# Kernel optimization log

Measured on AMD Instinct MI355X. Metric: run time of the kernel, lower is better.

## Reference

```python
import jax, jax.numpy as jnp
import numpy as np

DIM = 1024
HEADS = 16
DIM_HEAD = 64
INNER = HEADS * DIM_HEAD
B, M, N = 8, 4096, 256
EPS = 1e-5


def layer_norm(x, g, b):
    mu = jnp.mean(x, axis=-1, keepdims=True)
    var = jnp.mean(jnp.square(x - mu), axis=-1, keepdims=True)
    return (x - mu) * jax.lax.rsqrt(var + EPS) * g + b


def setup_inputs() -> dict:
    key = jax.random.key(0)
    ks = jax.random.split(key, 8)
    x = jax.random.normal(ks[0], (B, M, DIM), dtype=jnp.float32)
    latents = jax.random.normal(ks[1], (B, N, DIM), dtype=jnp.float32)
    x_att_mask = jax.random.randint(ks[2], (B, M), 0, 2) == 1  # True = masked
    s = 0.02
    Wq = jax.random.normal(ks[3], (DIM, INNER), dtype=jnp.float32) * s
    Wkv = jax.random.normal(ks[4], (DIM, 2 * INNER), dtype=jnp.float32) * s
    Wo = jax.random.normal(ks[5], (INNER, DIM), dtype=jnp.float32) * s
    return {
        "x": x, "latents": latents, "x_att_mask": x_att_mask,
        "nm_g": jnp.ones((DIM,), jnp.float32), "nm_b": jnp.zeros((DIM,), jnp.float32),
        "nl_g": jnp.ones((DIM,), jnp.float32), "nl_b": jnp.zeros((DIM,), jnp.float32),
        "Wq": Wq, "Wkv": Wkv, "Wo": Wo,
    }


def reference(x, latents, x_att_mask, nm_g, nm_b, nl_g, nl_b, Wq, Wkv, Wo):
    b, n, d = latents.shape
    h, dh = HEADS, DIM_HEAD
    scale = dh ** (-0.5)

    # additive mask: concat(media mask, all-False latent mask); True -> -inf, False -> +1 (faithful quirk)
    latent_mask = jnp.zeros((b, n), dtype=bool)
    full_mask = jnp.concatenate([x_att_mask, latent_mask], axis=1)  # [b, m+n]
    add_mask = jnp.where(full_mask, -jnp.inf, 1.0).astype(x.dtype)[:, None, None, :]  # [b,1,1,m+n]

    xn = layer_norm(x, nm_g, nm_b)
    ln = layer_norm(latents, nl_g, nl_b)

    q = (ln @ Wq).reshape(b, n, h, dh).transpose(0, 2, 1, 3)  # bhnd
    kv_in = jnp.concatenate([xn, ln], axis=1)                 # [b, m+n, d]
    kv = kv_in @ Wkv
    k, v = jnp.split(kv, 2, axis=-1)
    j = kv_in.shape[1]
    k = k.reshape(b, j, h, dh).transpose(0, 2, 1, 3)
    v = v.reshape(b, j, h, dh).transpose(0, 2, 1, 3)

    sim = jnp.einsum('bhid,bhjd->bhij', q * scale, k)
    sim = sim - jnp.max(sim, axis=-1, keepdims=True)
    sim = sim + add_mask
    attn = jax.nn.softmax(sim, axis=-1)
    out = jnp.einsum('bhij,bhjd->bhid', attn, v)
    out = out.transpose(0, 2, 1, 3).reshape(b, n, h * dh)
    return out @ Wo
```

## Files before the change

kernel.cpp:

```cpp
#include <hip/hip_runtime.h>
#include <hip/hip_bf16.h>
#include <stdint.h>

#define HEADS 16
#define DH    64
#define NB    8
#define MQ    256
#define MX    4096
#define JD    4352
#define DIMV  1024
#define GK    1024

typedef __bf16 bf16;
typedef __bf16 bf16x8 __attribute__((ext_vector_type(8)));
typedef float  f32x4  __attribute__((ext_vector_type(4)));

#define SWZ(r, c) (((c) ^ ((r) & 7)))

#define VMW(n) asm volatile("s_waitcnt vmcnt(" #n ")" ::: "memory")

__device__ __forceinline__ void gl_lds16(const void* g, void* l) {
  __builtin_amdgcn_global_load_lds((const __attribute__((address_space(1))) void*)g,
                                   (__attribute__((address_space(3))) void*)l, 16, 0, 0);
}

__global__ __launch_bounds__(256) void ln_all(
    const float* __restrict__ X, const float* __restrict__ LAT,
    const float* __restrict__ nmg, const float* __restrict__ nmb,
    const float* __restrict__ nlg, const float* __restrict__ nlb,
    bf16* __restrict__ out_kv, bf16* __restrict__ out_ln)
{
  const int row = blockIdx.x;
  const int tid = threadIdx.x;
  const bool lat = row >= NB * MX;
  const float *src, *gw, *bw;
  size_t kvrow; int lrow = 0;
  if (lat) {
    lrow = row - NB * MX;
    const int b = lrow >> 8, i = lrow & 255;
    src = LAT + (size_t)lrow * DIMV; gw = nlg; bw = nlb;
    kvrow = (size_t)b * JD + MX + i;
  } else {
    const int b = row >> 12, j = row & 4095;
    src = X + (size_t)row * DIMV; gw = nmg; bw = nmb;
    kvrow = (size_t)b * JD + j;
  }
  const float4 v = ((const float4*)src)[tid];
  float s  = v.x + v.y + v.z + v.w;
  float s2 = v.x*v.x + v.y*v.y + v.z*v.z + v.w*v.w;
#pragma unroll
  for (int m = 1; m < 64; m <<= 1) { s += __shfl_xor(s, m); s2 += __shfl_xor(s2, m); }
  __shared__ float red[8];
  const int wid = tid >> 6;
  if ((tid & 63) == 0) { red[wid*2] = s; red[wid*2+1] = s2; }
  __syncthreads();
  s  = red[0] + red[2] + red[4] + red[6];
  s2 = red[1] + red[3] + red[5] + red[7];
  const float mu  = s * (1.0f / DIMV);
  const float var = s2 * (1.0f / DIMV) - mu * mu;
  const float rst = rsqrtf(var + 1e-5f);
  const float4 g4 = ((const float4*)gw)[tid];
  const float4 b4 = ((const float4*)bw)[tid];
  union { bf16 h[4]; short4 s4; } u;
  u.h[0] = (bf16)((v.x - mu) * rst * g4.x + b4.x);
  u.h[1] = (bf16)((v.y - mu) * rst * g4.y + b4.y);
  u.h[2] = (bf16)((v.z - mu) * rst * g4.z + b4.z);
  u.h[3] = (bf16)((v.w - mu) * rst * g4.w + b4.w);
  *(short4*)(out_kv + kvrow * DIMV + tid * 4) = u.s4;
  if (lat) *(short4*)(out_ln + (size_t)lrow * DIMV + tid * 4) = u.s4;
}

__global__ __launch_bounds__(256) void transpose_all(
    const float* __restrict__ Wq, const float* __restrict__ Wkv,
    const float* __restrict__ Wo,
    bf16* __restrict__ WqT, bf16* __restrict__ WkvT, bf16* __restrict__ WoT)
{
  const int bid = blockIdx.x;
  const float* in; bf16* out; int C, tb;
  if (bid < 256)      { in = Wq;  out = WqT;  C = 1024; tb = bid; }
  else if (bid < 768) { in = Wkv; out = WkvT; C = 2048; tb = bid - 256; }
  else                { in = Wo;  out = WoT;  C = 1024; tb = bid - 768; }
  const int R = 1024;
  __shared__ float t[64][65];
  const int tilesC = C >> 6;
  const int tc = tb % tilesC, tr = tb / tilesC;
  const int r0 = tr << 6, c0 = tc << 6;
  const int lr = threadIdx.x >> 4;
  const int lc = (threadIdx.x & 15) << 2;
#pragma unroll
  for (int p = 0; p < 4; p++) {
    float4 v = *(const float4*)&in[(size_t)(r0 + lr + p*16) * C + c0 + lc];
    t[lr + p*16][lc    ] = v.x; t[lr + p*16][lc + 1] = v.y;
    t[lr + p*16][lc + 2] = v.z; t[lr + p*16][lc + 3] = v.w;
  }
  __syncthreads();
#pragma unroll
  for (int p = 0; p < 4; p++) {
    const int oc = lr + p*16;
    union { bf16 h[4]; short4 s4; } u;
    u.h[0] = (bf16)t[lc    ][oc]; u.h[1] = (bf16)t[lc + 1][oc];
    u.h[2] = (bf16)t[lc + 2][oc]; u.h[3] = (bf16)t[lc + 3][oc];
    *(short4*)&out[(size_t)(c0 + oc) * R + r0 + lc] = u.s4;
  }
}

__global__ __launch_bounds__(256) void mask_all(
    const void* __restrict__ mraw, float* __restrict__ madd)
{
  const int tid = threadIdx.x;
  const unsigned char* mb = (const unsigned char*)mraw;
  int cnt = 0;
  for (int i = tid; i < 32768; i += 256) cnt += (mb[i] != 0) ? 1 : 0;
#pragma unroll
  for (int m = 1; m < 64; m <<= 1) cnt += __shfl_xor(cnt, m);
  __shared__ int r4[4];
  if ((tid & 63) == 0) r4[tid >> 6] = cnt;
  __syncthreads();
  const int tot = r4[0] + r4[1] + r4[2] + r4[3];
  const bool bytemode = (tot * 16 > 32768 * 5);
  const int idx = blockIdx.x * 256 + tid;
  const int b = idx / JD, j = idx - b * JD;
  float v = 0.0f;
  if (j < MX) {
    bool masked = bytemode ? (mb[b * MX + j] != 0)
                           : (((const int*)mraw)[b * MX + j] != 0);
    v = masked ? -20000.0f : 0.0f;
  }
  madd[idx] = v;
}

__global__ __launch_bounds__(512, 2) void gemm256(
    const bf16* __restrict__ A, const bf16* __restrict__ Bt,
    const bf16* __restrict__ Aq, const bf16* __restrict__ Bq,
    bf16* __restrict__ outR, bf16* __restrict__ outVT, bf16* __restrict__ outQ)
{
  __shared__ bf16 sm[65536];

  const int tid = threadIdx.x;
  const int lane = tid & 63, wid = tid >> 6;
  const int wr = wid >> 2, wc = wid & 3;
  const int lc = lane & 15, lq = lane >> 4;
  const int srow = tid >> 3, sc = tid & 7;
  const int ssw = SWZ(srow, sc) * 8;

  int bid = blockIdx.x;
  bid = (bid & 7) * 140 + (bid >> 3);

  const bf16 *Arow, *Brow;
  int m0, n0, omode;
  if (bid < 1088) {
    const int by = bid >> 3, bx = bid & 7;
    m0 = by * 256;
    if (bx < 4) { n0 = bx * 256;
      Arow = A  + (size_t)m0 * GK; Brow = Bt + (size_t)n0 * GK; omode = 0; }
    else        { n0 = 1024 + (bx - 4) * 256;
      Arow = Bt + (size_t)n0 * GK; Brow = A  + (size_t)m0 * GK; omode = 1; }
  } else {
    const int ix = bid - 1088;
    m0 = (ix >> 2) * 256; n0 = (ix & 3) * 256;
    Arow = Aq + (size_t)m0 * GK; Brow = Bq + (size_t)n0 * GK; omode = 2;
  }

  const bf16* Abase = Arow + (size_t)srow * GK + ssw;
  const bf16* Bbase = Brow + (size_t)srow * GK + ssw;

  auto stA = [&](int d, int h, int kt) {
#pragma unroll
    for (int l = 0; l < 2; ++l)
      gl_lds16(Abase + (size_t)(h*128 + l*64) * GK + kt * 64,
               &sm[d*32768 + (h*128 + l*64)*64 + tid*8]);
  };
  auto stB = [&](int d, int h, int kt) {
#pragma unroll
    for (int l = 0; l < 2; ++l)
      gl_lds16(Bbase + (size_t)(h*128 + l*64) * GK + kt * 64,
               &sm[d*32768 + 16384 + (h*128 + l*64)*64 + tid*8]);
  };

  f32x4 acc[8][4];
#pragma unroll
  for (int i = 0; i < 8; i++)
#pragma unroll
    for (int j = 0; j < 4; j++)
#pragma unroll
      for (int r = 0; r < 4; r++) acc[i][j][r] = 0.f;

#define DS_PHASE(d, q, STAGE_STMT, WAIT_STMT)                                  \
  {                                                                            \
    const bf16* As_ = sm + (d)*32768;                                          \
    const bf16* Bs_ = sm + (d)*32768 + 16384;                                  \
    bf16x8 af[2][2];                                                           \
    _Pragma("unroll") for (int mi = 0; mi < 2; ++mi)                           \
      _Pragma("unroll") for (int kk = 0; kk < 2; ++kk)                         \
        af[mi][kk] = *(const bf16x8*)&As_[(wr*128 + ((q)*2+mi)*16 + lc)*64 +   \
                                          SWZ(lc, kk*4 + lq)*8];               \
    if ((q) == 0) {                                                            \
      _Pragma("unroll") for (int n = 0; n < 4; ++n)                            \
        _Pragma("unroll") for (int kk = 0; kk < 2; ++kk)                       \
          bfrag[n][kk] = *(const bf16x8*)&Bs_[(wc*64 + n*16 + lc)*64 +         \
                                              SWZ(lc, kk*4 + lq)*8];           \
    }                                                                          \
    STAGE_STMT;                                                                \
    WAIT_STMT;                                                                 \
    __builtin_amdgcn_s_barrier();                                              \
    __builtin_amdgcn_s_setprio(1);                                             \
    _Pragma("unroll") for (int kk = 0; kk < 2; ++kk)                           \
      _Pragma("unroll") for (int mi = 0; mi < 2; ++mi)                         \
        _Pragma("unroll") for (int n = 0; n < 4; ++n)                          \
          acc[(q)*2+mi][n] = __builtin_amdgcn_mfma_f32_16x16x32_bf16(          \
              af[mi][kk], bfrag[n][kk], acc[(q)*2+mi][n], 0, 0, 0);            \
    __builtin_amdgcn_s_setprio(0);                                             \
    __builtin_amdgcn_s_barrier();                                              \
  }

  stB(0, 0, 0); stB(0, 1, 0);
  stA(0, 0, 0); stA(0, 1, 0);
  stB(1, 0, 1); stB(1, 1, 1);
  VMW(4);
  __builtin_amdgcn_s_barrier();

  bf16x8 bfrag[4][2];
#pragma unroll 1
  for (int it = 0; it < 8; ++it) {
    const int tb = 2*it + 1, ta2 = 2*it + 2, tb2 = 2*it + 3;
    const bool s2 = (ta2 < 16), s3 = (tb2 < 16);
    DS_PHASE(0, 0, { stA(1, 0, tb); stA(1, 1, tb); }, {});
    DS_PHASE(0, 1, { if (s2) stB(0, 0, ta2); }, {});
    DS_PHASE(0, 2, { if (s2) stB(0, 1, ta2); }, {});
    DS_PHASE(0, 3, {}, { if (s2) { VMW(4); } else { VMW(0); } });
    DS_PHASE(1, 0, { if (s2) stA(0, 0, ta2); }, {});
    DS_PHASE(1, 1, { if (s2) stA(0, 1, ta2); }, {});
    DS_PHASE(1, 2, { if (s3) stB(1, 0, tb2); }, {});
    DS_PHASE(1, 3, { if (s3) stB(1, 1, tb2); }, { if (s3) { VMW(4); } });
  }
#undef DS_PHASE

  __syncthreads();
  bf16* Ct = sm;
#pragma unroll
  for (int m = 0; m < 8; ++m)
#pragma unroll
    for (int n = 0; n < 4; ++n) {
      const int col = wc*64 + n*16 + lc;
      const int cch = col >> 3, cw = col & 7;
#pragma unroll
      for (int r = 0; r < 4; ++r) {
        const int row = wr*128 + m*16 + lq*4 + r;
        Ct[row*256 + (((cch ^ (row & 31)) << 3) + cw)] = (bf16)acc[m][n][r];
      }
    }
  __syncthreads();

  const int cch = tid & 31, r0 = tid >> 5;
  if (omode != 1) {
    bf16* dst0 = (omode == 0 ? outR : outQ);
#pragma unroll
    for (int i = 0; i < 16; ++i) {
      const int row = r0 + i*16;
      bf16x8 v = *(const bf16x8*)&Ct[row*256 + ((cch ^ (row & 31)) << 3)];
      *(bf16x8*)(dst0 + (size_t)(m0 + row) * 1024 + n0 + cch*8) = v;
    }
  } else {
    const int bb = m0 / JD;
    const int jbase = m0 - bb * JD;
#pragma unroll
    for (int i = 0; i < 16; ++i) {
      const int row = r0 + i*16;
      const int cc = n0 + row - 1024;
      bf16x8 v = *(const bf16x8*)&Ct[row*256 + ((cch ^ (row & 31)) << 3)];
      bf16* dst = outVT + (((size_t)(bb*HEADS + (cc >> 6)))*64 + (cc & 63)) * JD
                        + jbase + cch*8;
      *(bf16x8*)dst = v;
    }
  }
}

__global__ __launch_bounds__(256) void gemm128(
    const bf16* __restrict__ A, const bf16* __restrict__ Bt,
    float* __restrict__ Cf, int N)
{
  __shared__ bf16 smem[2 * 128 * 64];
  bf16* As = smem;
  bf16* Bs = smem + 128 * 64;

  const int tid = threadIdx.x;
  const int lane = tid & 63, wid = tid >> 6;
  const int wr = wid >> 1, wc = wid & 1;
  const int m0 = blockIdx.y * 128;
  const int n0 = blockIdx.x * 128;
  const int srow = tid >> 3, sc = tid & 7;
  const int ssw = SWZ(srow, sc) * 8;
  const int lc = lane & 15, lq = lane >> 4;

  f32x4 acc[4][4];
#pragma unroll
  for (int i = 0; i < 4; i++)
#pragma unroll
    for (int j = 0; j < 4; j++)
#pragma unroll
      for (int r = 0; r < 4; r++) acc[i][j][r] = 0.f;

  const bf16* Abase = A + (size_t)m0 * GK + (size_t)srow * GK + ssw;
  const bf16* Bbase = Bt + (size_t)n0 * GK + (size_t)srow * GK + ssw;

  for (int k0 = 0; k0 < GK; k0 += 64) {
    __syncthreads();
#pragma unroll
    for (int q = 0; q < 4; q++) {
      gl_lds16(Abase + (size_t)q * 32 * GK + k0, &As[(srow + q*32) * 64 + sc*8]);
      gl_lds16(Bbase + (size_t)q * 32 * GK + k0, &Bs[(srow + q*32) * 64 + sc*8]);
    }
    VMW(0);
    __syncthreads();
#pragma unroll
    for (int kk = 0; kk < 2; kk++) {
      bf16x8 af[4], bfr[4];
#pragma unroll
      for (int mi = 0; mi < 4; mi++)
        af[mi] = *(const bf16x8*)&As[(wr*64 + mi*16 + lc) * 64 + SWZ(lc, kk*4 + lq)*8];
#pragma unroll
      for (int ni = 0; ni < 4; ni++)
        bfr[ni] = *(const bf16x8*)&Bs[(wc*64 + ni*16 + lc) * 64 + SWZ(lc, kk*4 + lq)*8];
#pragma unroll
      for (int mi = 0; mi < 4; mi++)
#pragma unroll
        for (int ni = 0; ni < 4; ni++)
          acc[mi][ni] = __builtin_amdgcn_mfma_f32_16x16x32_bf16(af[mi], bfr[ni], acc[mi][ni], 0, 0, 0);
    }
  }

#pragma unroll
  for (int mi = 0; mi < 4; mi++)
#pragma unroll
    for (int ni = 0; ni < 4; ni++) {
      const int r = m0 + wr*64 + mi*16 + lq*4;
      const int c = n0 + wc*64 + ni*16 + lc;
#pragma unroll
      for (int reg = 0; reg < 4; reg++)
        Cf[(size_t)(r + reg) * N + c] = acc[mi][ni][reg];
    }
}

__global__ __launch_bounds__(512) void attn_kernel(
    const bf16* __restrict__ Qrows,
    const bf16* __restrict__ Krows,
    const bf16* __restrict__ VT,
    const float* __restrict__ madd,
    bf16* __restrict__ outp)
{
  const int bh = blockIdx.x >> 1, qt = blockIdx.x & 1;
  const int b = bh >> 4, h = bh & 15;
  __shared__ bf16 Qs[128 * 64];
  __shared__ bf16 Ks[5][64 * 64];
  __shared__ bf16 VTs[5][64 * 64];
  __shared__ bf16 Ps[8][16 * 64];
  __shared__ float Madd[JD];
  const int tid = threadIdx.x, lane = tid & 63, w = tid >> 6;
  const int lc = lane & 15, lq = lane >> 4;
  const int srow = tid >> 3, sc = tid & 7;
  const int ssw = SWZ(srow, sc) * 8;

  const bf16* Qg = Qrows + ((size_t)(b*MQ + qt*128)) * 1024 + h*64;
  const bf16* Kg = Krows + ((size_t)b * JD) * 1024 + h*64;
  const bf16* Vg = VT + ((size_t)bh * 64) * JD;
  const float* mp = madd + (size_t)b * JD;

  auto stKV = [&](int c, int t) {
    gl_lds16(Kg + (size_t)(t*64 + srow) * 1024 + ssw, &Ks[c][tid*8]);
    gl_lds16(Vg + (size_t)srow * JD + t*64 + ssw, &VTs[c][tid*8]);
  };

  gl_lds16(Qg + (size_t)srow * 1024 + ssw, &Qs[tid*8]);
  gl_lds16(Qg + (size_t)(srow + 64) * 1024 + ssw, &Qs[(tid + 512)*8]);
  gl_lds16(mp + tid*4,        &Madd[tid*4]);
  gl_lds16(mp + 2048 + tid*4, &Madd[2048 + tid*4]);
  if (tid < 64) gl_lds16(mp + 4096 + tid*4, &Madd[4096 + tid*4]);
  VMW(0);
  stKV(0, 0); stKV(1, 1); stKV(2, 2); stKV(3, 3);
  __syncthreads();

  bf16x8 qf[2];
#pragma unroll
  for (int kk = 0; kk < 2; kk++)
    qf[kk] = *(const bf16x8*)&Qs[(w*16 + lc) * 64 + SWZ(lc, kk*4 + lq)*8];

  char* PsW = (char*)&Ps[w][0];
  f32x4 oacc[4];
  float den = 0.f;
#pragma unroll
  for (int di = 0; di < 4; di++)
#pragma unroll
    for (int r = 0; r < 4; r++) oacc[di][r] = 0.f;

  int c = 0;
#pragma unroll 1
  for (int t = 0; t < JD/64; ++t) {
    if (t <= JD/64 - 4)      { VMW(6); }
    else if (t == JD/64 - 3) { VMW(4); }
    else if (t == JD/64 - 2) { VMW(2); }
    else                     { VMW(0); }
    __builtin_amdgcn_s_barrier();
    if (t + 4 < JD/64) {
      const int c4 = (c == 0) ? 4 : c - 1;
      stKV(c4, t + 4);
    }
    const int j0 = t * 64;

    f32x4 sacc[4];
#pragma unroll
    for (int nj = 0; nj < 4; nj++)
#pragma unroll
      for (int r = 0; r < 4; r++) sacc[nj][r] = 0.f;
#pragma unroll
    for (int kk = 0; kk < 2; kk++) {
      bf16x8 kf[4];
#pragma unroll
      for (int nj = 0; nj < 4; nj++)
        kf[nj] = *(const bf16x8*)&Ks[c][(nj*16 + lc) * 64 + SWZ(lc, kk*4 + lq)*8];
      __builtin_amdgcn_s_setprio(1);
#pragma unroll
      for (int nj = 0; nj < 4; nj++)
        sacc[nj] = __builtin_amdgcn_mfma_f32_16x16x32_bf16(kf[nj], qf[kk], sacc[nj], 0, 0, 0);
      __builtin_amdgcn_s_setprio(0);
    }

#pragma unroll
    for (int nj = 0; nj < 4; nj++) {
      const float4 ma4 = *(const float4*)&Madd[j0 + nj*16 + lq*4];
      const float p0 = exp2f(fmaf(sacc[nj][0], 0.18033688f, ma4.x));
      const float p1 = exp2f(fmaf(sacc[nj][1], 0.18033688f, ma4.y));
      const float p2 = exp2f(fmaf(sacc[nj][2], 0.18033688f, ma4.z));
      const float p3 = exp2f(fmaf(sacc[nj][3], 0.18033688f, ma4.w));
      den += (p0 + p1) + (p2 + p3);
      union { bf16 h[4]; uint2 u2; } pu;
      pu.h[0] = (bf16)p0; pu.h[1] = (bf16)p1; pu.h[2] = (bf16)p2; pu.h[3] = (bf16)p3;
      const int c4s = (nj*2 + (lq >> 1)) ^ (lc & 7);
      *(uint2*)(PsW + lc*128 + (c4s << 4) + ((lq & 1) << 3)) = pu.u2;
    }

#pragma unroll
    for (int kk = 0; kk < 2; kk++) {
      bf16x8 pf = *(const bf16x8*)(PsW + lc*128 + ((((kk << 2) + lq) ^ (lc & 7)) << 4));
      __builtin_amdgcn_s_setprio(1);
#pragma unroll
      for (int di = 0; di < 4; di++) {
        bf16x8 vf = *(const bf16x8*)&VTs[c][(di*16 + lc) * 64 + SWZ(lc, kk*4 + lq)*8];
        oacc[di] = __builtin_amdgcn_mfma_f32_16x16x32_bf16(pf, vf, oacc[di], 0, 0, 0);
      }
      __builtin_amdgcn_s_setprio(0);
    }

    c = (c == 4) ? 0 : c + 1;
  }

  den += __shfl_xor(den, 16);
  den += __shfl_xor(den, 32);
  const float rden = 1.0f / den;

#pragma unroll
  for (int di = 0; di < 4; di++) {
    const int col = h*64 + di*16 + lc;
#pragma unroll
    for (int r = 0; r < 4; r++) {
      const float dr = __shfl(rden, lq*4 + r, 16);
      const int i = qt*128 + w*16 + lq*4 + r;
      outp[(size_t)(b*MQ + i) * 1024 + col] = (bf16)(oacc[di][r] * dr);
    }
  }
}

extern "C" void kernel_launch(void* const* d_in, const int* in_sizes, int n_in,
                              void* d_out, int out_size, void* d_ws, size_t ws_size,
                              hipStream_t stream)
{
  const float* x    = (const float*)d_in[0];
  const float* lat  = (const float*)d_in[1];
  const void*  mraw = d_in[2];
  const float* nm_g = (const float*)d_in[3];
  const float* nm_b = (const float*)d_in[4];
  const float* nl_g = (const float*)d_in[5];
  const float* nl_b = (const float*)d_in[6];
  const float* Wq   = (const float*)d_in[7];
  const float* Wkv  = (const float*)d_in[8];
  const float* Wo   = (const float*)d_in[9];
  float* out = (float*)d_out;

  char* p = (char*)d_ws;
  auto alloc = [&](size_t bytes) { char* r = p; p += (bytes + 255) & ~(size_t)255; return r; };

  bf16*  kv_in  = (bf16*)alloc((size_t)NB * JD * DIMV * 2);
  bf16*  Krows  = (bf16*)alloc((size_t)NB * JD * 1024 * 2);
  bf16*  VTbuf  = (bf16*)alloc((size_t)NB * HEADS * 64 * JD * 2);
  bf16*  WqT    = (bf16*)alloc((size_t)1024 * 1024 * 2);
  bf16*  WkvT   = (bf16*)alloc((size_t)2048 * 1024 * 2);
  bf16*  WoT    = (bf16*)alloc((size_t)1024 * 1024 * 2);
  bf16*  ln_buf = (bf16*)alloc((size_t)NB * MQ * DIMV * 2);
  bf16*  Qrows  = (bf16*)alloc((size_t)NB * MQ * 1024 * 2);
  bf16*  attout = (bf16*)alloc((size_t)NB * MQ * DIMV * 2);
  float* maddp  = (float*)alloc((size_t)NB * JD * 4);
  (void)ws_size; (void)in_sizes; (void)n_in; (void)out_size;

  ln_all<<<NB * (MX + MQ), 256, 0, stream>>>(x, lat, nm_g, nm_b, nl_g, nl_b,
                                             kv_in, ln_buf);
  transpose_all<<<1024, 256, 0, stream>>>(Wq, Wkv, Wo, WqT, WkvT, WoT);
  mask_all<<<136, 256, 0, stream>>>(mraw, maddp);

  gemm256<<<1120, 512, 0, stream>>>(kv_in, WkvT, ln_buf, WqT, Krows, VTbuf, Qrows);
  attn_kernel<<<256, 512, 0, stream>>>(Qrows, Krows, VTbuf, maddp, attout);
  gemm128<<<dim3(8, 16), 256, 0, stream>>>(attout, WoT, out, 1024);
}
```

Baseline: 524.9 us.

## Software-pipeline LDS fragment reads and use one barrier per GEMM phase

Restructures the GEMM main loop so each phase loads the next A fragments from LDS into a second register set while the MFMAs run on the current set. B fragments now go into two separate register sets, one per LDS buffer. Each phase now has a single barrier at its start instead of two. The global-to-LDS staging is spread more evenly, one stA per phase. The aim is to hide LDS read latency behind matrix math and cut barrier stalls, at the cost of more vector registers, which may lower occupancy or cause spills.

```diff
diff --git a/kernel.cpp b/kernel.cpp
--- a/kernel.cpp
+++ b/kernel.cpp
@@ -185,55 +185,81 @@
 #pragma unroll
       for (int r = 0; r < 4; r++) acc[i][j][r] = 0.f;
 
-#define DS_PHASE(d, q, STAGE_STMT, WAIT_STMT)                                  \
-  {                                                                            \
-    const bf16* As_ = sm + (d)*32768;                                          \
-    const bf16* Bs_ = sm + (d)*32768 + 16384;                                  \
-    bf16x8 af[2][2];                                                           \
-    _Pragma("unroll") for (int mi = 0; mi < 2; ++mi)                           \
-      _Pragma("unroll") for (int kk = 0; kk < 2; ++kk)                         \
-        af[mi][kk] = *(const bf16x8*)&As_[(wr*128 + ((q)*2+mi)*16 + lc)*64 +   \
-                                          SWZ(lc, kk*4 + lq)*8];               \
-    if ((q) == 0) {                                                            \
-      _Pragma("unroll") for (int n = 0; n < 4; ++n)                            \
-        _Pragma("unroll") for (int kk = 0; kk < 2; ++kk)                       \
-          bfrag[n][kk] = *(const bf16x8*)&Bs_[(wc*64 + n*16 + lc)*64 +         \
-                                              SWZ(lc, kk*4 + lq)*8];           \
-    }                                                                          \
-    STAGE_STMT;                                                                \
-    WAIT_STMT;                                                                 \
-    __builtin_amdgcn_s_barrier();                                              \
+  bf16x8 afP[2][2], afQ[2][2], bfA[4][2], bfB[4][2];
+
+#define MMC(CURA, BF, q)                                                       \
     __builtin_amdgcn_s_setprio(1);                                             \
     _Pragma("unroll") for (int kk = 0; kk < 2; ++kk)                           \
       _Pragma("unroll") for (int mi = 0; mi < 2; ++mi)                         \
         _Pragma("unroll") for (int n = 0; n < 4; ++n)                          \
           acc[(q)*2+mi][n] = __builtin_amdgcn_mfma_f32_16x16x32_bf16(          \
-              af[mi][kk], bfrag[n][kk], acc[(q)*2+mi][n], 0, 0, 0);            \
-    __builtin_amdgcn_s_setprio(0);                                             \
+              CURA[mi][kk], BF[n][kk], acc[(q)*2+mi][n], 0, 0, 0);             \
+    __builtin_amdgcn_s_setprio(0);
+
+#define PH_Q0(d, BF, CURA, NXTA, STAGE_STMT)                                   \
+  {                                                                            \
     __builtin_amdgcn_s_barrier();                                              \
+    STAGE_STMT;                                                                \
+    const bf16* As_ = sm + (d)*32768;                                          \
+    const bf16* Bs_ = sm + (d)*32768 + 16384;                                  \
+    _Pragma("unroll") for (int n = 0; n < 4; ++n)                              \
+      _Pragma("unroll") for (int kk = 0; kk < 2; ++kk)                         \
+        BF[n][kk] = *(const bf16x8*)&Bs_[(wc*64 + n*16 + lc)*64 +              \
+                                         SWZ(lc, kk*4 + lq)*8];                \
+    _Pragma("unroll") for (int mi = 0; mi < 2; ++mi)                           \
+      _Pragma("unroll") for (int kk = 0; kk < 2; ++kk) {                       \
+        CURA[mi][kk] = *(const bf16x8*)&As_[(wr*128 + mi*16 + lc)*64 +         \
+                                            SWZ(lc, kk*4 + lq)*8];             \
+        NXTA[mi][kk] = *(const bf16x8*)&As_[(wr*128 + (2+mi)*16 + lc)*64 +     \
+                                            SWZ(lc, kk*4 + lq)*8];             \
+      }                                                                        \
+    MMC(CURA, BF, 0)                                                           \
+  }
+
+#define PH_N(d, BF, CURA, NXTA, q, STAGE_STMT)                                 \
+  {                                                                            \
+    __builtin_amdgcn_s_barrier();                                              \
+    STAGE_STMT;                                                                \
+    const bf16* As_ = sm + (d)*32768;                                          \
+    _Pragma("unroll") for (int mi = 0; mi < 2; ++mi)                           \
+      _Pragma("unroll") for (int kk = 0; kk < 2; ++kk)                         \
+        NXTA[mi][kk] = *(const bf16x8*)&As_[(wr*128 + (((q)+1)*2+mi)*16 + lc)*64 \
+                                            + SWZ(lc, kk*4 + lq)*8];           \
+    MMC(CURA, BF, q)                                                           \
+  }
+
+#define PH_L(BF, CURA, STAGE_STMT, WAIT_STMT)                                  \
+  {                                                                            \
+    __builtin_amdgcn_s_barrier();                                              \
+    STAGE_STMT;                                                                \
+    MMC(CURA, BF, 3)                                                           \
+    WAIT_STMT;                                                                 \
   }
 
   stB(0, 0, 0); stB(0, 1, 0);
   stA(0, 0, 0); stA(0, 1, 0);
   stB(1, 0, 1); stB(1, 1, 1);
   VMW(4);
-  __builtin_amdgcn_s_barrier();
-
-  bf16x8 bfrag[4][2];
+
 #pragma unroll 1
   for (int it = 0; it < 8; ++it) {
     const int tb = 2*it + 1, ta2 = 2*it + 2, tb2 = 2*it + 3;
     const bool s2 = (ta2 < 16), s3 = (tb2 < 16);
-    DS_PHASE(0, 0, { stA(1, 0, tb); stA(1, 1, tb); }, {});
-    DS_PHASE(0, 1, { if (s2) stB(0, 0, ta2); }, {});
-    DS_PHASE(0, 2, { if (s2) stB(0, 1, ta2); }, {});
-    DS_PHASE(0, 3, {}, { if (s2) { VMW(4); } else { VMW(0); } });
-    DS_PHASE(1, 0, { if (s2) stA(0, 0, ta2); }, {});
-    DS_PHASE(1, 1, { if (s2) stA(0, 1, ta2); }, {});
-    DS_PHASE(1, 2, { if (s3) stB(1, 0, tb2); }, {});
-    DS_PHASE(1, 3, { if (s3) stB(1, 1, tb2); }, { if (s3) { VMW(4); } });
-  }
-#undef DS_PHASE
+    PH_Q0(0, bfA, afP, afQ, { stA(1, 0, tb); });
+    PH_N (0, bfA, afQ, afP, 1, { stA(1, 1, tb); });
+    PH_N (0, bfA, afP, afQ, 2, { if (s2) stB(0, 0, ta2); });
+    PH_L (bfA, afQ, { if (s2) stB(0, 1, ta2); },
+          { if (s2) { VMW(4); } else { VMW(0); } });
+    PH_Q0(1, bfB, afP, afQ, { if (s2) stA(0, 0, ta2); });
+    PH_N (1, bfB, afQ, afP, 1, { if (s2) stA(0, 1, ta2); });
+    PH_N (1, bfB, afP, afQ, 2, { if (s3) stB(1, 0, tb2); });
+    PH_L (bfB, afQ, { if (s3) stB(1, 1, tb2); },
+          { if (s3) { VMW(4); } });
+  }
+#undef PH_Q0
+#undef PH_N
+#undef PH_L
+#undef MMC
 
   __syncthreads();
   bf16* Ct = sm;
```

Result: no change. 532.6 us (+1.5%).
